# Kernel optimization log

Hardware: AMD Instinct MI355X
Metric: run time of the kernel (lower is better)

Reference implementation:

```python
import jax, jax.numpy as jnp
import numpy as np

B, S, D, H = 4, 2048, 1024, 16
HD = D // H


def setup_inputs() -> dict:
    key = jax.random.key(0)
    ks = jax.random.split(key, 5)
    scale = 1.0 / np.sqrt(D)
    inp = {
        "x": jax.random.normal(ks[0], (B, S, D), dtype=jnp.float32),
        # causal mask; masked_fill where mask == 0
        "mask": jnp.tril(jnp.ones((S, S), dtype=jnp.int32))[None, None, :, :],
        "Wq": jax.random.normal(ks[1], (D, D), dtype=jnp.float32) * scale,
        "bq": jnp.zeros((D,), dtype=jnp.float32),
        "Wk": jax.random.normal(ks[2], (D, D), dtype=jnp.float32) * scale,
        "bk": jnp.zeros((D,), dtype=jnp.float32),
        "Wv": jax.random.normal(ks[3], (D, D), dtype=jnp.float32) * scale,
        "bv": jnp.zeros((D,), dtype=jnp.float32),
        "Wo": jax.random.normal(ks[4], (D, D), dtype=jnp.float32) * scale,
        "bo": jnp.zeros((D,), dtype=jnp.float32),
    }
    return inp


def reference(x, mask, Wq, bq, Wk, bk, Wv, bv, Wo, bo):
    # weights stored [in, out]: y = x @ W + b (equivalent to torch Linear)
    def split_heads(t):  # [B,S,D] -> [B,H,S,HD]
        return t.reshape(B, S, H, HD).transpose(0, 2, 1, 3)

    q = split_heads(x @ Wq + bq)
    k = split_heads(x @ Wk + bk)
    v = split_heads(x @ Wv + bv)

    scores = jnp.einsum("bhqd,bhkd->bhqk", q, k) / jnp.sqrt(jnp.float32(HD))
    scores = jnp.where(mask == 0, -jnp.inf, scores)
    weights = jax.nn.softmax(scores, axis=-1)  # dropout_prob == 0, no dropout
    z = jnp.einsum("bhqk,bhkd->bhqd", weights, v)
    z = z.transpose(0, 2, 1, 3).reshape(B, S, D)
    return z @ Wo + bo
```

## Files before the change

kernel.cpp:

```cpp
#include <hip/hip_runtime.h>
#include <cmath>


#define BB 4
#define SS 2048
#define DD 1024
#define HH 16
#define HD 64
#define MM (BB * SS)

typedef __bf16 bf16x8 __attribute__((ext_vector_type(8)));
typedef float f32x4 __attribute__((ext_vector_type(4)));
typedef unsigned short ushort4e __attribute__((ext_vector_type(4)));
typedef unsigned short ushort8e __attribute__((ext_vector_type(8)));

#define SCALE_Q 0.18033688011112042f
#define EXP2(x) __builtin_amdgcn_exp2f(x)
#define M0 24.0f

__device__ __forceinline__ void gload_lds16(const void* g, void* l) {
    __builtin_amdgcn_global_load_lds((const __attribute__((address_space(1))) void*)g,
                                     (__attribute__((address_space(3))) void*)l, 16, 0, 0);
}

__device__ __forceinline__ unsigned short f2bf(float f) {
    union { float f; unsigned u; } v; v.f = f;
    unsigned r = v.u + 0x7fff + ((v.u >> 16) & 1);
    return (unsigned short)(r >> 16);
}

__global__ __launch_bounds__(256) void cast_f32_bf16(const float* __restrict__ in,
                                                     unsigned short* __restrict__ out) {
    const int i = blockIdx.x * 256 + threadIdx.x;
    const float4 v = ((const float4*)in)[i];
    ushort4e o;
    o[0] = f2bf(v.x); o[1] = f2bf(v.y); o[2] = f2bf(v.z); o[3] = f2bf(v.w);
    *(ushort4e*)&out[(size_t)i * 4] = o;
}

__global__ __launch_bounds__(256) void wtrans(const float* __restrict__ W0, const float* __restrict__ W1,
                                              const float* __restrict__ W2, const float* __restrict__ W3,
                                              unsigned short* __restrict__ O0, unsigned short* __restrict__ O1,
                                              unsigned short* __restrict__ O2, unsigned short* __restrict__ O3) {
    __shared__ unsigned short T[64][72];
    const float* W = blockIdx.z == 0 ? W0 : blockIdx.z == 1 ? W1 : blockIdx.z == 2 ? W2 : W3;
    unsigned short* O = blockIdx.z == 0 ? O0 : blockIdx.z == 1 ? O1 : blockIdx.z == 2 ? O2 : O3;
    const int k0 = blockIdx.x * 64, n0 = blockIdx.y * 64;
    const int t = threadIdx.x;
#pragma unroll
    for (int i = 0; i < 4; i++) {
        const int r = (t >> 4) + 16 * i, c4 = (t & 15) * 4;
        const float4 w = *(const float4*)&W[(size_t)(k0 + r) * DD + n0 + c4];
        T[c4 + 0][r] = f2bf(w.x); T[c4 + 1][r] = f2bf(w.y);
        T[c4 + 2][r] = f2bf(w.z); T[c4 + 3][r] = f2bf(w.w);
    }
    __syncthreads();
    const int nl = t >> 2, kc = (t & 3) * 16;
    const ushort8e a = *(const ushort8e*)&T[nl][kc];
    const ushort8e b = *(const ushort8e*)&T[nl][kc + 8];
    *(ushort8e*)&O[(size_t)(n0 + nl) * DD + k0 + kc] = a;
    *(ushort8e*)&O[(size_t)(n0 + nl) * DD + k0 + kc + 8] = b;
}

template <int MODE>
__global__ __launch_bounds__(512, 4) void gemm128(const unsigned short* __restrict__ A,
                                                  const unsigned short* __restrict__ Bt,
                                                  const float* __restrict__ b0,
                                                  const float* __restrict__ b1,
                                                  const float* __restrict__ b2,
                                                  void* __restrict__ o0,
                                                  void* __restrict__ o1,
                                                  void* __restrict__ o2) {
    __shared__ char smem[73728];

    const int tid = threadIdx.x, lane = tid & 63, w = tid >> 6;
    const int wm = w >> 2, wn = w & 3;
    const int g = lane >> 4, l15 = lane & 15;
    const int m0 = blockIdx.x * 128, n0 = blockIdx.y * 256;

    f32x4 acc[4][4];
#pragma unroll
    for (int i = 0; i < 4; i++)
#pragma unroll
        for (int j = 0; j < 4; j++) acc[i][j] = (f32x4){0.f, 0.f, 0.f, 0.f};

    auto stage = [&](int bb, int kt) {
        const int k0 = kt * 32;
        char* abase = smem + bb * 8192;
        char* bbase = smem + 24576 + bb * 16384;
        {
            const int o = tid * 16;
            const int r = o >> 6;
            const int cc = ((o >> 4) & 3) ^ ((r >> 1) & 3);
            gload_lds16(A + (size_t)(m0 + r) * DD + k0 + cc * 8, abase + w * 1024);
        }
#pragma unroll
        for (int ld = 0; ld < 2; ld++) {
            const int o = ld * 8192 + tid * 16;
            const int r = o >> 6;
            const int cc = ((o >> 4) & 3) ^ ((r >> 1) & 3);
            gload_lds16(Bt + (size_t)(n0 + r) * DD + k0 + cc * 8, bbase + ld * 8192 + w * 1024);
        }
    };

    stage(0, 0); stage(1, 1);
    asm volatile("s_waitcnt vmcnt(3)" ::: "memory");
    __builtin_amdgcn_s_barrier();

    for (int kt = 0; kt < 32; kt++) {
        const int bb = kt % 3;
        const char* abase = smem + bb * 8192;
        const char* bbase = smem + 24576 + bb * 16384;
        bf16x8 afr[4], bfr[4];
#pragma unroll
        for (int mf = 0; mf < 4; mf++) {
            const int r = wm * 64 + mf * 16 + l15;
            afr[mf] = *(const bf16x8*)(abase + r * 64 + ((g ^ ((r >> 1) & 3)) << 4));
        }
#pragma unroll
        for (int nf = 0; nf < 4; nf++) {
            const int r = wn * 64 + nf * 16 + l15;
            bfr[nf] = *(const bf16x8*)(bbase + r * 64 + ((g ^ ((r >> 1) & 3)) << 4));
        }
        if (kt <= 29) stage((kt + 2) % 3, kt + 2);
        __builtin_amdgcn_sched_barrier(0);
        __builtin_amdgcn_s_setprio(1);
#pragma unroll
        for (int mf = 0; mf < 4; mf++)
#pragma unroll
            for (int nf = 0; nf < 4; nf++)
                acc[mf][nf] = __builtin_amdgcn_mfma_f32_16x16x32_bf16(afr[mf], bfr[nf], acc[mf][nf], 0, 0, 0);
        __builtin_amdgcn_s_setprio(0);
        __builtin_amdgcn_sched_barrier(0);
        if (kt <= 29) asm volatile("s_waitcnt vmcnt(3)" ::: "memory");
        else asm volatile("s_waitcnt vmcnt(0)" ::: "memory");
        __builtin_amdgcn_s_barrier();
    }

    if (MODE == 1) {
        float* op = (float*)o0;
#pragma unroll
        for (int nf = 0; nf < 4; nf++) {
            const int col = n0 + wn * 64 + nf * 16 + l15;
            const float bv_ = b0[col];
#pragma unroll
            for (int mf = 0; mf < 4; mf++) {
                const int mrow0 = m0 + wm * 64 + mf * 16 + g * 4;
                const f32x4 v = acc[mf][nf];
#pragma unroll
                for (int r = 0; r < 4; r++) op[(size_t)(mrow0 + r) * DD + col] = v[r] + bv_;
            }
        }
    } else {
        const int proj = n0 >> 10;
        const int nbase = n0 & 1023;
        const float* bias = proj == 0 ? b0 : proj == 1 ? b1 : b2;
        unsigned short* op = (unsigned short*)(proj == 0 ? o0 : proj == 1 ? o1 : o2);
        if (proj < 2) {
            const float scale = proj == 0 ? SCALE_Q : 1.0f;
            char* ws = smem + w * 8192;
            const int mbase = m0 + wm * 64;
            const int b_ = mbase >> 11, s0 = mbase & 2047;
            const int h = (nbase + wn * 64) >> 6;
#pragma unroll
            for (int nf = 0; nf < 4; nf++) {
                const int col = nf * 16 + l15;
                const float bv_ = bias[h * 64 + col];
#pragma unroll
                for (int mf = 0; mf < 4; mf++) {
                    const f32x4 v = acc[mf][nf];
#pragma unroll
                    for (int r = 0; r < 4; r++) {
                        const int lm = mf * 16 + g * 4 + r;
                        *(unsigned short*)(ws + lm * 128 + (((col >> 3) ^ (lm & 7)) << 4) + (col & 7) * 2) =
                            f2bf((v[r] + bv_) * scale);
                    }
                }
            }
            asm volatile("s_waitcnt lgkmcnt(0)" ::: "memory");
            __builtin_amdgcn_sched_barrier(0);
#pragma unroll
            for (int rr = 0; rr < 8; rr++) {
                const int lm = rr * 8 + (lane & 7);
                const int c16 = lane >> 3;
                const ushort8e val = *(const ushort8e*)(ws + lm * 128 + ((c16 ^ (lm & 7)) << 4));
                *(ushort8e*)&op[(((size_t)(b_ * HH + h)) * SS + s0 + lm) * HD + c16 * 8] = val;
            }
        } else {
#pragma unroll
            for (int nf = 0; nf < 4; nf++) {
                const int col = nbase + wn * 64 + nf * 16 + l15;
                const float bv_ = bias[col];
                const int h = col >> 6, hd = col & 63;
#pragma unroll
                for (int mf = 0; mf < 4; mf++) {
                    const int m = m0 + wm * 64 + mf * 16 + g * 4;
                    const int b_ = m >> 11, s = m & 2047;
                    const int u = s & 63;
                    const int pos = (s & ~63) + (u >> 5) * 32 + ((u >> 2) & 3) * 8 + ((u >> 4) & 1) * 4;
                    const f32x4 v = acc[mf][nf];
                    ushort4e o4;
#pragma unroll
                    for (int r = 0; r < 4; r++) o4[r] = f2bf(v[r] + bv_);
                    *(ushort4e*)&op[(((size_t)(b_ * HH + h)) * HD + hd) * SS + pos] = o4;
                }
            }
        }
    }
}

__global__ __launch_bounds__(256) void attn(const unsigned short* __restrict__ Q,
                                            const unsigned short* __restrict__ K,
                                            const unsigned short* __restrict__ Vt,
                                            unsigned short* __restrict__ Z) {
    __shared__ unsigned short Ks[2][4096];
    __shared__ unsigned short Vs[2][4096];

    const int tid = threadIdx.x, lane = tid & 63, w = tid >> 6;
    const int g = lane >> 4, l15 = lane & 15;
    const int bh = blockIdx.x & 63, tpair = blockIdx.x >> 6;
    const int b = bh >> 4, h = bh & 15;
    const unsigned short* Qb = Q + (size_t)bh * SS * HD;
    const unsigned short* Kb = K + (size_t)bh * SS * HD;
    const unsigned short* Vb = Vt + (size_t)bh * HD * SS;

    const int ob0 = w * 2048, ob1 = w * 2048 + 1024;
    auto stage = [&](int bb, int kt) {
        const int k0 = kt * 64;
#pragma unroll
        for (int i = 0; i < 2; i++) {
            const int ob = i ? ob1 : ob0;
            const int o = ob + lane * 16;
            const int row = o >> 7;
            const int c = ((o >> 4) & 7) ^ (row & 7);
            gload_lds16(Kb + (size_t)(k0 + row) * HD + c * 8, (char*)&Ks[bb][0] + ob);
            gload_lds16(Vb + (size_t)row * SS + k0 + c * 8, (char*)&Vs[bb][0] + ob);
        }
    };

#pragma unroll
    for (int half = 0; half < 2; half++) {
        const int t = half ? (15 - tpair) : tpair;
        const int q0 = t * 128;
        const int qw = q0 + w * 32;

        bf16x8 qf[2][2];
#pragma unroll
        for (int nf = 0; nf < 2; nf++)
#pragma unroll
            for (int ks = 0; ks < 2; ks++)
                qf[nf][ks] = *(const bf16x8*)&Qb[(size_t)(qw + nf * 16 + l15) * HD + ks * 32 + g * 8];

        float ps[2] = {0.f, 0.f};
        f32x4 oacc[4][2];
#pragma unroll
        for (int mh = 0; mh < 4; mh++)
#pragma unroll
            for (int nf = 0; nf < 2; nf++) oacc[mh][nf] = (f32x4){0.f, 0.f, 0.f, 0.f};

        const int nt = 2 * t + 2;
        int cur = 0;
        stage(0, 0);
        __syncthreads();
#pragma unroll 2
        for (int kt = 0; kt < nt; kt++) {
            const int k0 = kt * 64;
            if (kt + 1 < nt) stage(cur ^ 1, kt + 1);
            if (k0 <= qw + 31) {
                f32x4 sacc[4][2];
#pragma unroll
                for (int mf = 0; mf < 4; mf++)
#pragma unroll
                    for (int nf = 0; nf < 2; nf++) sacc[mf][nf] = (f32x4){0.f, 0.f, 0.f, 0.f};
                __builtin_amdgcn_s_setprio(1);
#pragma unroll
                for (int ks = 0; ks < 2; ks++) {
                    bf16x8 af[4];
#pragma unroll
                    for (int mf = 0; mf < 4; mf++) {
                        const int row = mf * 16 + l15;
                        const int c = (ks * 4 + g) ^ (row & 7);
                        af[mf] = *(const bf16x8*)((const char*)&Ks[cur][0] + row * 128 + c * 16);
                    }
#pragma unroll
                    for (int mf = 0; mf < 4; mf++)
#pragma unroll
                        for (int nf = 0; nf < 2; nf++)
                            sacc[mf][nf] = __builtin_amdgcn_mfma_f32_16x16x32_bf16(af[mf], qf[nf][ks], sacc[mf][nf], 0, 0, 0);
                }
                __builtin_amdgcn_s_setprio(0);
                if (k0 + 63 > qw) {
#pragma unroll
                    for (int mf = 0; mf < 4; mf++)
#pragma unroll
                        for (int nf = 0; nf < 2; nf++)
#pragma unroll
                            for (int r = 0; r < 4; r++) {
                                const int key = k0 + mf * 16 + g * 4 + r;
                                const int q = qw + nf * 16 + l15;
                                if (key > q) sacc[mf][nf][r] = -INFINITY;
                            }
                }
                bf16x8 pb[2][2];
#pragma unroll
                for (int nf = 0; nf < 2; nf++) {
                    float pv[16];
#pragma unroll
                    for (int mf = 0; mf < 4; mf++)
#pragma unroll
                        for (int r = 0; r < 4; r++) {
                            const float p = EXP2(sacc[mf][nf][r] - M0);
                            pv[mf * 4 + r] = p;
                            ps[nf] += p;
                        }
#pragma unroll
                    for (int j = 0; j < 4; j++) {
                        pb[nf][0][j] = (__bf16)pv[j];
                        pb[nf][0][4 + j] = (__bf16)pv[4 + j];
                        pb[nf][1][j] = (__bf16)pv[8 + j];
                        pb[nf][1][4 + j] = (__bf16)pv[12 + j];
                    }
                }
                __builtin_amdgcn_s_setprio(1);
#pragma unroll
                for (int ks = 0; ks < 2; ks++) {
#pragma unroll
                    for (int mh = 0; mh < 4; mh++) {
                        const int row = mh * 16 + l15;
                        const int c = (ks * 4 + g) ^ (row & 7);
                        const bf16x8 va = *(const bf16x8*)((const char*)&Vs[cur][0] + row * 128 + c * 16);
#pragma unroll
                        for (int nf = 0; nf < 2; nf++)
                            oacc[mh][nf] = __builtin_amdgcn_mfma_f32_16x16x32_bf16(va, pb[nf][ks], oacc[mh][nf], 0, 0, 0);
                    }
                }
                __builtin_amdgcn_s_setprio(0);
            }
            __syncthreads();
            cur ^= 1;
        }

#pragma unroll
        for (int nf = 0; nf < 2; nf++) {
            float l = ps[nf];
            l += __shfl_xor(l, 16);
            l += __shfl_xor(l, 32);
            const float inv = 1.f / l;
            const int qg = qw + nf * 16 + l15;
#pragma unroll
            for (int mh = 0; mh < 4; mh++) {
                ushort4e o;
#pragma unroll
                for (int r = 0; r < 4; r++) o[r] = f2bf(oacc[mh][nf][r] * inv);
                *(ushort4e*)&Z[((size_t)(b * SS + qg)) * DD + h * HD + mh * 16 + g * 4] = o;
            }
        }
    }
}

extern "C" void kernel_launch(void* const* d_in, const int* in_sizes, int n_in,
                              void* d_out, int out_size, void* d_ws, size_t ws_size,
                              hipStream_t stream) {
    const float* x  = (const float*)d_in[0];
    const float* Wq = (const float*)d_in[2];
    const float* bq = (const float*)d_in[3];
    const float* Wk = (const float*)d_in[4];
    const float* bk = (const float*)d_in[5];
    const float* Wv = (const float*)d_in[6];
    const float* bv = (const float*)d_in[7];
    const float* Wo = (const float*)d_in[8];
    const float* bo = (const float*)d_in[9];
    float* out = (float*)d_out;

    unsigned short* xb  = (unsigned short*)d_ws;
    unsigned short* wqt = xb  + (size_t)MM * DD;
    unsigned short* wkt = wqt + (size_t)DD * DD;
    unsigned short* wvt = wkt + (size_t)DD * DD;
    unsigned short* wot = wvt + (size_t)DD * DD;
    unsigned short* qb  = wot + (size_t)DD * DD;
    unsigned short* kb  = qb  + (size_t)MM * DD;
    unsigned short* vtb = kb  + (size_t)MM * DD;
    unsigned short* zb  = vtb + (size_t)MM * DD;

    const dim3 blk(256), blk2(512);
    cast_f32_bf16<<<dim3(MM * DD / 1024), blk, 0, stream>>>(x, xb);
    wtrans<<<dim3(16, 16, 4), blk, 0, stream>>>(Wq, Wk, Wv, Wo, wqt, wkt, wvt, wot);

    gemm128<0><<<dim3(MM / 128, 3 * DD / 256), blk2, 0, stream>>>(xb, wqt, bq, bk, bv, qb, kb, vtb);

    attn<<<dim3(512), blk, 0, stream>>>(qb, kb, vtb, zb);

    gemm128<1><<<dim3(MM / 128, DD / 256), blk2, 0, stream>>>(zb, wot, bo, bo, bo, out, out, out);
}
```

Before: 253.6 us.

## Split attention key tiles across two wave groups and shrink output GEMM tile

The attention kernel moves to 512 threads, with two wave groups each handling half of every 64-key tile. Their partial O and row sums are reduced through shared memory at the end. The row-sum is now computed with an MFMA against a ones vector, and the softmax offset is folded into the score accumulator's initial value. The output projection GEMM is templated on BN and run with 128-wide N tiles, which doubles the block count for better CU fill at the cost of some reuse. Risks are the extra reduction sync and LDS traffic in attention.

After: 238.5 us. 6.0% less time.

```diff
diff --git a/kernel.cpp b/kernel.cpp
--- a/kernel.cpp
+++ b/kernel.cpp
@@ -21,6 +21,13 @@
 __device__ __forceinline__ void gload_lds16(const void* g, void* l) {
     __builtin_amdgcn_global_load_lds((const __attribute__((address_space(1))) void*)g,
                                      (__attribute__((address_space(3))) void*)l, 16, 0, 0);
+}
+
+template <int N>
+__device__ __forceinline__ void vwait() {
+    if constexpr (N == 0) asm volatile("s_waitcnt vmcnt(0)" ::: "memory");
+    else if constexpr (N == 2) asm volatile("s_waitcnt vmcnt(2)" ::: "memory");
+    else if constexpr (N == 3) asm volatile("s_waitcnt vmcnt(3)" ::: "memory");
 }
 
 __device__ __forceinline__ unsigned short f2bf(float f) {
@@ -62,64 +69,68 @@
     *(ushort8e*)&O[(size_t)(n0 + nl) * DD + k0 + kc + 8] = b;
 }
 
-template <int MODE>
-__global__ __launch_bounds__(512, 4) void gemm128(const unsigned short* __restrict__ A,
-                                                  const unsigned short* __restrict__ Bt,
-                                                  const float* __restrict__ b0,
-                                                  const float* __restrict__ b1,
-                                                  const float* __restrict__ b2,
-                                                  void* __restrict__ o0,
-                                                  void* __restrict__ o1,
-                                                  void* __restrict__ o2) {
-    __shared__ char smem[73728];
+template <int MODE, int BN>
+__global__ __launch_bounds__(512, 4) void gemmk(const unsigned short* __restrict__ A,
+                                                const unsigned short* __restrict__ Bt,
+                                                const float* __restrict__ b0,
+                                                const float* __restrict__ b1,
+                                                const float* __restrict__ b2,
+                                                void* __restrict__ o0,
+                                                void* __restrict__ o1,
+                                                void* __restrict__ o2) {
+    constexpr int ASLOT = 8192;
+    constexpr int BSLOT = BN * 64;
+    constexpr int NF = BN / 64;
+    constexpr int WCOL = BN / 4;
+    constexpr int LPS = 1 + BN / 128;
+    __shared__ char smem[3 * (ASLOT + BSLOT)];
 
     const int tid = threadIdx.x, lane = tid & 63, w = tid >> 6;
     const int wm = w >> 2, wn = w & 3;
     const int g = lane >> 4, l15 = lane & 15;
-    const int m0 = blockIdx.x * 128, n0 = blockIdx.y * 256;
-
-    f32x4 acc[4][4];
+    const int m0 = blockIdx.x * 128, n0 = blockIdx.y * BN;
+
+    f32x4 acc[4][NF];
 #pragma unroll
     for (int i = 0; i < 4; i++)
 #pragma unroll
-        for (int j = 0; j < 4; j++) acc[i][j] = (f32x4){0.f, 0.f, 0.f, 0.f};
+        for (int j = 0; j < NF; j++) acc[i][j] = (f32x4){0.f, 0.f, 0.f, 0.f};
 
     auto stage = [&](int bb, int kt) {
         const int k0 = kt * 32;
-        char* abase = smem + bb * 8192;
-        char* bbase = smem + 24576 + bb * 16384;
         {
             const int o = tid * 16;
             const int r = o >> 6;
             const int cc = ((o >> 4) & 3) ^ ((r >> 1) & 3);
-            gload_lds16(A + (size_t)(m0 + r) * DD + k0 + cc * 8, abase + w * 1024);
-        }
-#pragma unroll
-        for (int ld = 0; ld < 2; ld++) {
+            gload_lds16(A + (size_t)(m0 + r) * DD + k0 + cc * 8, smem + bb * ASLOT + w * 1024);
+        }
+#pragma unroll
+        for (int ld = 0; ld < BN / 128; ld++) {
             const int o = ld * 8192 + tid * 16;
             const int r = o >> 6;
             const int cc = ((o >> 4) & 3) ^ ((r >> 1) & 3);
-            gload_lds16(Bt + (size_t)(n0 + r) * DD + k0 + cc * 8, bbase + ld * 8192 + w * 1024);
+            gload_lds16(Bt + (size_t)(n0 + r) * DD + k0 + cc * 8,
+                        smem + 3 * ASLOT + bb * BSLOT + ld * 8192 + w * 1024);
         }
     };
 
     stage(0, 0); stage(1, 1);
-    asm volatile("s_waitcnt vmcnt(3)" ::: "memory");
+    vwait<LPS>();
     __builtin_amdgcn_s_barrier();
 
     for (int kt = 0; kt < 32; kt++) {
         const int bb = kt % 3;
-        const char* abase = smem + bb * 8192;
-        const char* bbase = smem + 24576 + bb * 16384;
-        bf16x8 afr[4], bfr[4];
+        const char* abase = smem + bb * ASLOT;
+        const char* bbase = smem + 3 * ASLOT + bb * BSLOT;
+        bf16x8 afr[4], bfr[NF];
 #pragma unroll
         for (int mf = 0; mf < 4; mf++) {
             const int r = wm * 64 + mf * 16 + l15;
             afr[mf] = *(const bf16x8*)(abase + r * 64 + ((g ^ ((r >> 1) & 3)) << 4));
         }
 #pragma unroll
-        for (int nf = 0; nf < 4; nf++) {
-            const int r = wn * 64 + nf * 16 + l15;
+        for (int nf = 0; nf < NF; nf++) {
+            const int r = wn * WCOL + nf * 16 + l15;
             bfr[nf] = *(const bf16x8*)(bbase + r * 64 + ((g ^ ((r >> 1) & 3)) << 4));
         }
         if (kt <= 29) stage((kt + 2) % 3, kt + 2);
@@ -128,20 +139,19 @@
 #pragma unroll
         for (int mf = 0; mf < 4; mf++)
 #pragma unroll
-            for (int nf = 0; nf < 4; nf++)
+            for (int nf = 0; nf < NF; nf++)
                 acc[mf][nf] = __builtin_amdgcn_mfma_f32_16x16x32_bf16(afr[mf], bfr[nf], acc[mf][nf], 0, 0, 0);
         __builtin_amdgcn_s_setprio(0);
         __builtin_amdgcn_sched_barrier(0);
-        if (kt <= 29) asm volatile("s_waitcnt vmcnt(3)" ::: "memory");
-        else asm volatile("s_waitcnt vmcnt(0)" ::: "memory");
+        if (kt <= 29) vwait<LPS>(); else vwait<0>();
         __builtin_amdgcn_s_barrier();
     }
 
     if (MODE == 1) {
         float* op = (float*)o0;
 #pragma unroll
-        for (int nf = 0; nf < 4; nf++) {
-            const int col = n0 + wn * 64 + nf * 16 + l15;
+        for (int nf = 0; nf < NF; nf++) {
+            const int col = n0 + wn * WCOL + nf * 16 + l15;
             const float bv_ = b0[col];
 #pragma unroll
             for (int mf = 0; mf < 4; mf++) {
@@ -161,9 +171,9 @@
             char* ws = smem + w * 8192;
             const int mbase = m0 + wm * 64;
             const int b_ = mbase >> 11, s0 = mbase & 2047;
-            const int h = (nbase + wn * 64) >> 6;
-#pragma unroll
-            for (int nf = 0; nf < 4; nf++) {
+            const int h = (nbase + wn * WCOL) >> 6;
+#pragma unroll
+            for (int nf = 0; nf < NF; nf++) {
                 const int col = nf * 16 + l15;
                 const float bv_ = bias[h * 64 + col];
 #pragma unroll
@@ -188,8 +198,8 @@
             }
         } else {
 #pragma unroll
-            for (int nf = 0; nf < 4; nf++) {
-                const int col = nbase + wn * 64 + nf * 16 + l15;
+            for (int nf = 0; nf < NF; nf++) {
+                const int col = nbase + wn * WCOL + nf * 16 + l15;
                 const float bv_ = bias[col];
                 const int h = col >> 6, hd = col & 63;
 #pragma unroll
@@ -209,14 +219,14 @@
     }
 }
 
-__global__ __launch_bounds__(256) void attn(const unsigned short* __restrict__ Q,
-                                            const unsigned short* __restrict__ K,
-                                            const unsigned short* __restrict__ Vt,
-                                            unsigned short* __restrict__ Z) {
-    __shared__ unsigned short Ks[2][4096];
-    __shared__ unsigned short Vs[2][4096];
+__global__ __launch_bounds__(512, 4) void attn(const unsigned short* __restrict__ Q,
+                                               const unsigned short* __restrict__ K,
+                                               const unsigned short* __restrict__ Vt,
+                                               unsigned short* __restrict__ Z) {
+    __shared__ char smem[33280];
 
     const int tid = threadIdx.x, lane = tid & 63, w = tid >> 6;
+    const int grp = w >> 2, wq = w & 3;
     const int g = lane >> 4, l15 = lane & 15;
     const int bh = blockIdx.x & 63, tpair = blockIdx.x >> 6;
     const int b = bh >> 4, h = bh & 15;
@@ -224,25 +234,24 @@
     const unsigned short* Kb = K + (size_t)bh * SS * HD;
     const unsigned short* Vb = Vt + (size_t)bh * HD * SS;
 
-    const int ob0 = w * 2048, ob1 = w * 2048 + 1024;
+    bf16x8 ones;
+#pragma unroll
+    for (int j = 0; j < 8; j++) ones[j] = (__bf16)1.0f;
+
     auto stage = [&](int bb, int kt) {
         const int k0 = kt * 64;
-#pragma unroll
-        for (int i = 0; i < 2; i++) {
-            const int ob = i ? ob1 : ob0;
-            const int o = ob + lane * 16;
-            const int row = o >> 7;
-            const int c = ((o >> 4) & 7) ^ (row & 7);
-            gload_lds16(Kb + (size_t)(k0 + row) * HD + c * 8, (char*)&Ks[bb][0] + ob);
-            gload_lds16(Vb + (size_t)row * SS + k0 + c * 8, (char*)&Vs[bb][0] + ob);
-        }
+        const int o = tid * 16;
+        const int row = o >> 7;
+        const int c = ((o >> 4) & 7) ^ (row & 7);
+        gload_lds16(Kb + (size_t)(k0 + row) * HD + c * 8, smem + bb * 8192 + w * 1024);
+        gload_lds16(Vb + (size_t)row * SS + k0 + c * 8, smem + 16384 + bb * 8192 + w * 1024);
     };
 
 #pragma unroll
     for (int half = 0; half < 2; half++) {
         const int t = half ? (15 - tpair) : tpair;
         const int q0 = t * 128;
-        const int qw = q0 + w * 32;
+        const int qw = q0 + wq * 32;
 
         bf16x8 qf[2][2];
 #pragma unroll
@@ -251,88 +260,78 @@
             for (int ks = 0; ks < 2; ks++)
                 qf[nf][ks] = *(const bf16x8*)&Qb[(size_t)(qw + nf * 16 + l15) * HD + ks * 32 + g * 8];
 
-        float ps[2] = {0.f, 0.f};
-        f32x4 oacc[4][2];
-#pragma unroll
-        for (int mh = 0; mh < 4; mh++)
-#pragma unroll
-            for (int nf = 0; nf < 2; nf++) oacc[mh][nf] = (f32x4){0.f, 0.f, 0.f, 0.f};
+        f32x4 lacc[2], oacc[4][2];
+#pragma unroll
+        for (int nf = 0; nf < 2; nf++) {
+            lacc[nf] = (f32x4){0.f, 0.f, 0.f, 0.f};
+#pragma unroll
+            for (int mh = 0; mh < 4; mh++) oacc[mh][nf] = (f32x4){0.f, 0.f, 0.f, 0.f};
+        }
 
         const int nt = 2 * t + 2;
         int cur = 0;
         stage(0, 0);
         __syncthreads();
-#pragma unroll 2
         for (int kt = 0; kt < nt; kt++) {
             const int k0 = kt * 64;
             if (kt + 1 < nt) stage(cur ^ 1, kt + 1);
-            if (k0 <= qw + 31) {
-                f32x4 sacc[4][2];
-#pragma unroll
-                for (int mf = 0; mf < 4; mf++)
-#pragma unroll
-                    for (int nf = 0; nf < 2; nf++) sacc[mf][nf] = (f32x4){0.f, 0.f, 0.f, 0.f};
+            const int kbase = k0 + grp * 32;
+            if (kbase <= qw + 31) {
+                f32x4 sacc[2][2];
+#pragma unroll
+                for (int mf = 0; mf < 2; mf++)
+#pragma unroll
+                    for (int nf = 0; nf < 2; nf++) sacc[mf][nf] = (f32x4){-M0, -M0, -M0, -M0};
                 __builtin_amdgcn_s_setprio(1);
 #pragma unroll
                 for (int ks = 0; ks < 2; ks++) {
-                    bf16x8 af[4];
-#pragma unroll
-                    for (int mf = 0; mf < 4; mf++) {
-                        const int row = mf * 16 + l15;
+                    bf16x8 af[2];
+#pragma unroll
+                    for (int mf = 0; mf < 2; mf++) {
+                        const int row = grp * 32 + mf * 16 + l15;
                         const int c = (ks * 4 + g) ^ (row & 7);
-                        af[mf] = *(const bf16x8*)((const char*)&Ks[cur][0] + row * 128 + c * 16);
+                        af[mf] = *(const bf16x8*)(smem + cur * 8192 + row * 128 + c * 16);
                     }
 #pragma unroll
-                    for (int mf = 0; mf < 4; mf++)
+                    for (int mf = 0; mf < 2; mf++)
 #pragma unroll
                         for (int nf = 0; nf < 2; nf++)
                             sacc[mf][nf] = __builtin_amdgcn_mfma_f32_16x16x32_bf16(af[mf], qf[nf][ks], sacc[mf][nf], 0, 0, 0);
                 }
                 __builtin_amdgcn_s_setprio(0);
-                if (k0 + 63 > qw) {
-#pragma unroll
-                    for (int mf = 0; mf < 4; mf++)
+                if (kbase + 31 > qw) {
+#pragma unroll
+                    for (int mf = 0; mf < 2; mf++)
 #pragma unroll
                         for (int nf = 0; nf < 2; nf++)
 #pragma unroll
                             for (int r = 0; r < 4; r++) {
-                                const int key = k0 + mf * 16 + g * 4 + r;
+                                const int key = kbase + mf * 16 + g * 4 + r;
                                 const int q = qw + nf * 16 + l15;
                                 if (key > q) sacc[mf][nf][r] = -INFINITY;
                             }
                 }
-                bf16x8 pb[2][2];
+                bf16x8 pb[2];
 #pragma unroll
                 for (int nf = 0; nf < 2; nf++) {
-                    float pv[16];
-#pragma unroll
-                    for (int mf = 0; mf < 4; mf++)
-#pragma unroll
-                        for (int r = 0; r < 4; r++) {
-                            const float p = EXP2(sacc[mf][nf][r] - M0);
-                            pv[mf * 4 + r] = p;
-                            ps[nf] += p;
-                        }
-#pragma unroll
-                    for (int j = 0; j < 4; j++) {
-                        pb[nf][0][j] = (__bf16)pv[j];
-                        pb[nf][0][4 + j] = (__bf16)pv[4 + j];
-                        pb[nf][1][j] = (__bf16)pv[8 + j];
-                        pb[nf][1][4 + j] = (__bf16)pv[12 + j];
-                    }
-                }
+#pragma unroll
+                    for (int mf = 0; mf < 2; mf++)
+#pragma unroll
+                        for (int r = 0; r < 4; r++)
+                            pb[nf][mf * 4 + r] = (__bf16)EXP2(sacc[mf][nf][r]);
+                }
+#pragma unroll
+                for (int nf = 0; nf < 2; nf++)
+                    lacc[nf] = __builtin_amdgcn_mfma_f32_16x16x32_bf16(ones, pb[nf], lacc[nf], 0, 0, 0);
                 __builtin_amdgcn_s_setprio(1);
 #pragma unroll
-                for (int ks = 0; ks < 2; ks++) {
-#pragma unroll
-                    for (int mh = 0; mh < 4; mh++) {
-                        const int row = mh * 16 + l15;
-                        const int c = (ks * 4 + g) ^ (row & 7);
-                        const bf16x8 va = *(const bf16x8*)((const char*)&Vs[cur][0] + row * 128 + c * 16);
-#pragma unroll
-                        for (int nf = 0; nf < 2; nf++)
-                            oacc[mh][nf] = __builtin_amdgcn_mfma_f32_16x16x32_bf16(va, pb[nf][ks], oacc[mh][nf], 0, 0, 0);
-                    }
+                for (int mh = 0; mh < 4; mh++) {
+                    const int row = mh * 16 + l15;
+                    const int c = (grp * 4 + g) ^ (row & 7);
+                    const bf16x8 va = *(const bf16x8*)(smem + 16384 + cur * 8192 + row * 128 + c * 16);
+#pragma unroll
+                    for (int nf = 0; nf < 2; nf++)
+                        oacc[mh][nf] = __builtin_amdgcn_mfma_f32_16x16x32_bf16(va, pb[nf], oacc[mh][nf], 0, 0, 0);
                 }
                 __builtin_amdgcn_s_setprio(0);
             }
@@ -340,21 +339,43 @@
             cur ^= 1;
         }
 
-#pragma unroll
-        for (int nf = 0; nf < 2; nf++) {
-            float l = ps[nf];
-            l += __shfl_xor(l, 16);
-            l += __shfl_xor(l, 32);
-            const float inv = 1.f / l;
-            const int qg = qw + nf * 16 + l15;
-#pragma unroll
-            for (int mh = 0; mh < 4; mh++) {
-                ushort4e o;
-#pragma unroll
-                for (int r = 0; r < 4; r++) o[r] = f2bf(oacc[mh][nf][r] * inv);
-                *(ushort4e*)&Z[((size_t)(b * SS + qg)) * DD + h * HD + mh * 16 + g * 4] = o;
-            }
-        }
+        float* Ored = (float*)smem;
+        float* lred = (float*)(smem + 32768);
+        if (grp == 1) {
+#pragma unroll
+            for (int nf = 0; nf < 2; nf++) {
+                const int q = wq * 32 + nf * 16 + l15;
+                lred[q] = lacc[nf][0];
+#pragma unroll
+                for (int mh = 0; mh < 4; mh++)
+#pragma unroll
+                    for (int r = 0; r < 4; r++) {
+                        const int hd = mh * 16 + g * 4 + r;
+                        Ored[hd * 128 + (q ^ (((hd >> 2) & 7) << 3))] = oacc[mh][nf][r];
+                    }
+            }
+        }
+        __syncthreads();
+        if (grp == 0) {
+#pragma unroll
+            for (int nf = 0; nf < 2; nf++) {
+                const int q = wq * 32 + nf * 16 + l15;
+                const float l = lacc[nf][0] + lred[q];
+                const float inv = 1.f / l;
+                const int qg = qw + nf * 16 + l15;
+#pragma unroll
+                for (int mh = 0; mh < 4; mh++) {
+                    ushort4e o4;
+#pragma unroll
+                    for (int r = 0; r < 4; r++) {
+                        const int hd = mh * 16 + g * 4 + r;
+                        o4[r] = f2bf((oacc[mh][nf][r] + Ored[hd * 128 + (q ^ (((hd >> 2) & 7) << 3))]) * inv);
+                    }
+                    *(ushort4e*)&Z[((size_t)(b * SS + qg)) * DD + h * HD + mh * 16 + g * 4] = o4;
+                }
+            }
+        }
+        __syncthreads();
     }
 }
 
@@ -386,9 +407,9 @@
     cast_f32_bf16<<<dim3(MM * DD / 1024), blk, 0, stream>>>(x, xb);
     wtrans<<<dim3(16, 16, 4), blk, 0, stream>>>(Wq, Wk, Wv, Wo, wqt, wkt, wvt, wot);
 
-    gemm128<0><<<dim3(MM / 128, 3 * DD / 256), blk2, 0, stream>>>(xb, wqt, bq, bk, bv, qb, kb, vtb);
-
-    attn<<<dim3(512), blk, 0, stream>>>(qb, kb, vtb, zb);
-
-    gemm128<1><<<dim3(MM / 128, DD / 256), blk2, 0, stream>>>(zb, wot, bo, bo, bo, out, out, out);
-}
+    gemmk<0, 256><<<dim3(MM / 128, 3 * DD / 256), blk2, 0, stream>>>(xb, wqt, bq, bk, bv, qb, kb, vtb);
+
+    attn<<<dim3(512), blk2, 0, stream>>>(qb, kb, vtb, zb);
+
+    gemmk<1, 128><<<dim3(MM / 128, DD / 128), blk2, 0, stream>>>(zb, wot, bo, bo, bo, out, out, out);
+}
```
